# Kernel tuning notes

Hardware: AMD Instinct MI355X
Metric: run time of the kernel (lower is better)

The kernel has to match this reference:

```python
import jax, jax.numpy as jnp
import numpy as np

B, T, C = 4, 2048, 1024
H, D = 16, 64  # num_heads, head_dim
WINDOW = 256


def setup_inputs() -> dict:
    key = jax.random.key(0)
    k_x, k_qkv, k_proj, k_qb, k_pb = jax.random.split(key, 5)
    x = jax.random.normal(k_x, (B, T, C), dtype=jnp.float32)
    # xavier-uniform-ish init for qkv weight (as in _reset_parameters)
    lim_qkv = float(np.sqrt(6.0 / (C + 3 * C)))
    qkv_w = jax.random.uniform(k_qkv, (3 * C, C), minval=-lim_qkv, maxval=lim_qkv, dtype=jnp.float32)
    qkv_b = jax.random.normal(k_qb, (3 * C,), dtype=jnp.float32) * 0.02
    lim_p = float(np.sqrt(1.0 / C))
    proj_w = jax.random.uniform(k_proj, (C, C), minval=-lim_p, maxval=lim_p, dtype=jnp.float32)
    proj_b = jax.random.normal(k_pb, (C,), dtype=jnp.float32) * 0.02
    # windowed causal mask: attend to j iff j <= i and i - j < WINDOW
    i = jnp.arange(T)[:, None]
    j = jnp.arange(T)[None, :]
    attn_mask = (j <= i) & (i - j < WINDOW)  # [T, T] bool
    return {"x": x, "attn_mask": attn_mask, "qkv_w": qkv_w, "qkv_b": qkv_b,
            "proj_w": proj_w, "proj_b": proj_b}


def reference(x, attn_mask, qkv_w, qkv_b, proj_w, proj_b):
    qkv = (x @ qkv_w.T + qkv_b).reshape(B, T, 3, H, D)
    qkv = jnp.transpose(qkv, (2, 0, 3, 1, 4))
    q, k, v = qkv[0], qkv[1], qkv[2]
    scale = 1.0 / jnp.sqrt(jnp.asarray(D, dtype=q.dtype))
    scores = jnp.einsum('bhqd,bhkd->bhqk', q, k) * scale  # [B,H,T,T]
    neg = jnp.asarray(jnp.finfo(scores.dtype).min, dtype=scores.dtype)
    scores = jnp.where(attn_mask[None, None], scores, neg)
    attn = jax.nn.softmax(scores, axis=-1)
    out = jnp.einsum('bhqk,bhkd->bhqd', attn, v)  # [B,H,T,D]
    out = jnp.transpose(out, (0, 2, 1, 3)).reshape(B, T, C)
    out = out @ proj_w.T + proj_b
    return out
```

## Files before the change

### kernel.cpp

```cpp
#include <hip/hip_runtime.h>

#define BB 4
#define TT 2048
#define CC 1024
#define HH 16
#define DD 64
#define WIN 256

typedef __attribute__((ext_vector_type(8))) short short8;
typedef __attribute__((ext_vector_type(4))) float floatx4;
typedef unsigned short u16;

typedef __attribute__((address_space(3))) void lds_void;
typedef const __attribute__((address_space(1))) void g_void;

__device__ __forceinline__ void gl_lds16(const u16* g, u16* l) {
    __builtin_amdgcn_global_load_lds((g_void*)g, (lds_void*)l, 16, 0, 0);
}

__device__ __forceinline__ float bf2f(u16 u) {
    union { unsigned int i; float f; } v; v.i = ((unsigned int)u) << 16; return v.f;
}
__device__ __forceinline__ u16 f2bf(float f) {
    union { float f; unsigned int i; } v; v.f = f;
    unsigned int x = v.i;
    x += ((x >> 16) & 1u) + 0x7FFFu;
    return (u16)(x >> 16);
}

__global__ void cvt_all(const float* __restrict__ x, const float* __restrict__ qw,
                        const float* __restrict__ pw,
                        u16* __restrict__ xb, u16* __restrict__ wb, u16* __restrict__ pwb) {
    int bid = blockIdx.x;
    const float* src; u16* dst; int off;
    if (bid < 4096)      { src = x;  dst = xb;  off = bid; }
    else if (bid < 5632) { src = qw; dst = wb;  off = bid - 4096; }
    else                 { src = pw; dst = pwb; off = bid - 5632; }
    int i = (off * 256 + (int)threadIdx.x) * 8;
    float4 a = *(const float4*)(src + i);
    float4 b = *(const float4*)(src + i + 4);
    u16 o[8] = { f2bf(a.x), f2bf(a.y), f2bf(a.z), f2bf(a.w),
                 f2bf(b.x), f2bf(b.y), f2bf(b.z), f2bf(b.w) };
    *(uint4*)(dst + i) = *(const uint4*)o;
}

__global__ __launch_bounds__(256) void gemm_qk(
    const u16* __restrict__ A, const u16* __restrict__ Bw,
    const float* __restrict__ bias,
    u16* __restrict__ Qb, u16* __restrict__ Kb)
{
    const int K = CC;
    __shared__ u16 As[4096];
    __shared__ u16 Bs[4096];
    const int tid = threadIdx.x;
    const int wave = tid >> 6, lane = tid & 63;
    const int wm = wave >> 1, wn = wave & 1;
    const int quad = lane >> 4, l15 = lane & 15;
    const int bN = blockIdx.x * 128, bM = blockIdx.y * 128;

    const int srow0 = wave * 16 + (lane >> 2);
    const int srow1 = (wave + 4) * 16 + (lane >> 2);
    const int schunk = ((lane & 3) ^ ((lane >> 3) & 3)) * 8;
    const u16* gA0 = A + (size_t)(bM + srow0) * K + schunk;
    const u16* gA1 = A + (size_t)(bM + srow1) * K + schunk;
    const u16* gB0 = Bw + (size_t)(bN + srow0) * K + schunk;
    const u16* gB1 = Bw + (size_t)(bN + srow1) * K + schunk;
    u16* lA0 = &As[wave * 512];
    u16* lA1 = &As[(wave + 4) * 512];
    u16* lB0 = &Bs[wave * 512];
    u16* lB1 = &Bs[(wave + 4) * 512];

    const int rdoff = l15 * 32 + ((quad ^ ((l15 >> 1) & 3)) * 8);

    floatx4 acc[4][4] = {};

    for (int k0 = 0; k0 < K; k0 += 32) {
        __syncthreads();
        gl_lds16(gA0 + k0, lA0);
        gl_lds16(gA1 + k0, lA1);
        gl_lds16(gB0 + k0, lB0);
        gl_lds16(gB1 + k0, lB1);
        __syncthreads();
        short8 af[4], bf[4];
#pragma unroll
        for (int i = 0; i < 4; ++i) {
            af[i] = *(const short8*)&As[(wm * 4 + i) * 512 + rdoff];
            bf[i] = *(const short8*)&Bs[(wn * 4 + i) * 512 + rdoff];
        }
#pragma unroll
        for (int mi = 0; mi < 4; ++mi)
#pragma unroll
            for (int ni = 0; ni < 4; ++ni)
                acc[mi][ni] = __builtin_amdgcn_mfma_f32_16x16x32_bf16(af[mi], bf[ni], acc[mi][ni], 0, 0, 0);
    }

#pragma unroll
    for (int mi = 0; mi < 4; ++mi)
#pragma unroll
        for (int ni = 0; ni < 4; ++ni) {
            int col = bN + wn * 64 + ni * 16 + l15;
            float bv = bias[col];
            int which = col >> 10, rem = col & 1023;
            int h = rem >> 6, d = rem & 63;
            int row0 = bM + wm * 64 + mi * 16 + quad * 4;
            int b = row0 >> 11, t0 = row0 & 2047;
            u16* dst = which == 0 ? Qb : Kb;
#pragma unroll
            for (int rg = 0; rg < 4; ++rg)
                dst[(((size_t)(b * HH + h)) * TT + t0 + rg) * DD + d] = f2bf(acc[mi][ni][rg] + bv);
        }
}

__global__ __launch_bounds__(256) void gemm_v(
    const u16* __restrict__ A, const u16* __restrict__ Bw,
    const float* __restrict__ bias,
    u16* __restrict__ Vtg)
{
    const int K = CC;
    __shared__ u16 As[4096];
    __shared__ u16 Bs[4096];
    const int tid = threadIdx.x;
    const int wave = tid >> 6, lane = tid & 63;
    const int wm = wave >> 1, wn = wave & 1;
    const int quad = lane >> 4, l15 = lane & 15;
    const int bN = 2048 + blockIdx.x * 128, bM = blockIdx.y * 128;

    const int srow0 = wave * 16 + (lane >> 2);
    const int srow1 = (wave + 4) * 16 + (lane >> 2);
    const int schunk = ((lane & 3) ^ ((lane >> 3) & 3)) * 8;
    const u16* gA0 = A + (size_t)(bM + srow0) * K + schunk;
    const u16* gA1 = A + (size_t)(bM + srow1) * K + schunk;
    const u16* gB0 = Bw + (size_t)(bN + srow0) * K + schunk;
    const u16* gB1 = Bw + (size_t)(bN + srow1) * K + schunk;
    u16* lA0 = &As[wave * 512];
    u16* lA1 = &As[(wave + 4) * 512];
    u16* lB0 = &Bs[wave * 512];
    u16* lB1 = &Bs[(wave + 4) * 512];

    const int rdoff = l15 * 32 + ((quad ^ ((l15 >> 1) & 3)) * 8);

    floatx4 acc[4][4] = {};

    for (int k0 = 0; k0 < K; k0 += 32) {
        __syncthreads();
        gl_lds16(gA0 + k0, lA0);
        gl_lds16(gA1 + k0, lA1);
        gl_lds16(gB0 + k0, lB0);
        gl_lds16(gB1 + k0, lB1);
        __syncthreads();
        short8 af[4], bf[4];
#pragma unroll
        for (int i = 0; i < 4; ++i) {
            af[i] = *(const short8*)&As[(wm * 4 + i) * 512 + rdoff];
            bf[i] = *(const short8*)&Bs[(wn * 4 + i) * 512 + rdoff];
        }
#pragma unroll
        for (int mi = 0; mi < 4; ++mi)
#pragma unroll
            for (int ni = 0; ni < 4; ++ni)
                acc[mi][ni] = __builtin_amdgcn_mfma_f32_16x16x32_bf16(bf[ni], af[mi], acc[mi][ni], 0, 0, 0);
    }

#pragma unroll
    for (int mi = 0; mi < 4; ++mi)
#pragma unroll
        for (int ni = 0; ni < 4; ++ni) {
            int col0 = bN + wn * 64 + ni * 16 + quad * 4;
            int row = bM + wm * 64 + mi * 16 + l15;
            int b = row >> 11, t = row & 2047;
#pragma unroll
            for (int rg = 0; rg < 4; ++rg) {
                int c = col0 + rg;
                int h = (c & 1023) >> 6, d = c & 63;
                float v = acc[mi][ni][rg] + bias[c];
                Vtg[(((size_t)(b * HH + h)) * DD + d) * TT + t] = f2bf(v);
            }
        }
}

__global__ __launch_bounds__(256) void gemm_proj(
    const u16* __restrict__ A, const u16* __restrict__ Bw,
    const float* __restrict__ bias, float* __restrict__ Out)
{
    const int K = CC;
    __shared__ u16 As[4096];
    __shared__ u16 Bs[4096];
    const int tid = threadIdx.x;
    const int wave = tid >> 6, lane = tid & 63;
    const int wm = wave >> 1, wn = wave & 1;
    const int quad = lane >> 4, l15 = lane & 15;
    const int bN = blockIdx.x * 128, bM = blockIdx.y * 128;

    const int srow0 = wave * 16 + (lane >> 2);
    const int srow1 = (wave + 4) * 16 + (lane >> 2);
    const int schunk = ((lane & 3) ^ ((lane >> 3) & 3)) * 8;
    const u16* gA0 = A + (size_t)(bM + srow0) * K + schunk;
    const u16* gA1 = A + (size_t)(bM + srow1) * K + schunk;
    const u16* gB0 = Bw + (size_t)(bN + srow0) * K + schunk;
    const u16* gB1 = Bw + (size_t)(bN + srow1) * K + schunk;
    u16* lA0 = &As[wave * 512];
    u16* lA1 = &As[(wave + 4) * 512];
    u16* lB0 = &Bs[wave * 512];
    u16* lB1 = &Bs[(wave + 4) * 512];

    const int rdoff = l15 * 32 + ((quad ^ ((l15 >> 1) & 3)) * 8);

    floatx4 acc[4][4] = {};

    for (int k0 = 0; k0 < K; k0 += 32) {
        __syncthreads();
        gl_lds16(gA0 + k0, lA0);
        gl_lds16(gA1 + k0, lA1);
        gl_lds16(gB0 + k0, lB0);
        gl_lds16(gB1 + k0, lB1);
        __syncthreads();
        short8 af[4], bf[4];
#pragma unroll
        for (int i = 0; i < 4; ++i) {
            af[i] = *(const short8*)&As[(wm * 4 + i) * 512 + rdoff];
            bf[i] = *(const short8*)&Bs[(wn * 4 + i) * 512 + rdoff];
        }
#pragma unroll
        for (int mi = 0; mi < 4; ++mi)
#pragma unroll
            for (int ni = 0; ni < 4; ++ni)
                acc[mi][ni] = __builtin_amdgcn_mfma_f32_16x16x32_bf16(af[mi], bf[ni], acc[mi][ni], 0, 0, 0);
    }

#pragma unroll
    for (int mi = 0; mi < 4; ++mi)
#pragma unroll
        for (int ni = 0; ni < 4; ++ni) {
            int col = bN + wn * 64 + ni * 16 + l15;
            float bv = bias[col];
#pragma unroll
            for (int rg = 0; rg < 4; ++rg) {
                int row = bM + wm * 64 + mi * 16 + quad * 4 + rg;
                Out[(size_t)row * CC + col] = acc[mi][ni][rg] + bv;
            }
        }
}

__global__ __launch_bounds__(256) void attn_mfma(
    const u16* __restrict__ Qb, const u16* __restrict__ Kb, const u16* __restrict__ Vtg,
    u16* __restrict__ Y)
{
    __shared__ __align__(16) u16 Ks[4096];
    __shared__ __align__(16) u16 Vs[4096];
    __shared__ __align__(16) u16 Ps[4][16][72];

    const int tid = threadIdx.x;
    const int wave = tid >> 6, lane = tid & 63;
    const int quad = lane >> 4, l15 = lane & 15;
    const int q0 = blockIdx.x * 64;
    const int bh = blockIdx.y;
    const int b = bh >> 4, h = bh & 15;
    const u16* Qp = Qb + (size_t)bh * TT * DD;
    const u16* Kp = Kb + (size_t)bh * TT * DD;
    const u16* Vp = Vtg + (size_t)bh * DD * TT;
    const int qw = q0 + wave * 16;

    const int lrow = lane >> 3;
    const int lchunk = ((lane & 7) ^ lrow) << 3;
    const int s0 = wave * 2, s1 = wave * 2 + 1;

    short8 qf[2];
    qf[0] = *(const short8*)&Qp[(size_t)(qw + l15) * DD + quad * 8];
    qf[1] = *(const short8*)&Qp[(size_t)(qw + l15) * DD + 32 + quad * 8];

    float m_i = -1e30f, l_i = 0.f;
    floatx4 Oacc[4] = {};

    const int swz = l15 & 7;
    const int kb = (q0 >= WIN) ? (q0 - WIN) : 0;
    for (int j0 = kb; j0 < q0 + 64; j0 += 64) {
        __syncthreads();
        gl_lds16(&Kp[(size_t)(j0 + s0 * 8 + lrow) * DD + lchunk], &Ks[s0 * 512]);
        gl_lds16(&Kp[(size_t)(j0 + s1 * 8 + lrow) * DD + lchunk], &Ks[s1 * 512]);
        gl_lds16(&Vp[(size_t)(s0 * 8 + lrow) * TT + j0 + lchunk], &Vs[s0 * 512]);
        gl_lds16(&Vp[(size_t)(s1 * 8 + lrow) * TT + j0 + lchunk], &Vs[s1 * 512]);
        __syncthreads();

        floatx4 Sacc[4] = {};
#pragma unroll
        for (int ks = 0; ks < 2; ++ks)
#pragma unroll
            for (int kt = 0; kt < 4; ++kt) {
                short8 kf = *(const short8*)&Ks[(kt * 16 + l15) * 64 + (((ks * 4 + quad) ^ swz) << 3)];
                Sacc[kt] = __builtin_amdgcn_mfma_f32_16x16x32_bf16(kf, qf[ks], Sacc[kt], 0, 0, 0);
            }

        const int q = qw + l15;
        float mc = -1e30f;
#pragma unroll
        for (int kt = 0; kt < 4; ++kt)
#pragma unroll
            for (int r = 0; r < 4; ++r) {
                int j = j0 + kt * 16 + quad * 4 + r;
                float s = (j <= q && (q - j) < WIN) ? Sacc[kt][r] * 0.125f : -1e30f;
                Sacc[kt][r] = s;
                mc = fmaxf(mc, s);
            }
        mc = fmaxf(mc, __shfl_xor(mc, 16, 64));
        mc = fmaxf(mc, __shfl_xor(mc, 32, 64));

        float mn = fmaxf(m_i, mc);
        float alpha = __expf(m_i - mn);
        m_i = mn;

        float rs = 0.f;
#pragma unroll
        for (int kt = 0; kt < 4; ++kt) {
            u16 pk[4];
#pragma unroll
            for (int r = 0; r < 4; ++r) {
                float s = Sacc[kt][r];
                float p = (s > -1e29f) ? __expf(s - m_i) : 0.f;
                rs += p;
                pk[r] = f2bf(p);
            }
            *(uint2*)&Ps[wave][l15][kt * 16 + quad * 4] = *(const uint2*)pk;
        }
        rs += __shfl_xor(rs, 16, 64);
        rs += __shfl_xor(rs, 32, 64);
        l_i = l_i * alpha + rs;
#pragma unroll
        for (int dt = 0; dt < 4; ++dt)
#pragma unroll
            for (int r = 0; r < 4; ++r) Oacc[dt][r] *= alpha;

#pragma unroll
        for (int ks = 0; ks < 2; ++ks) {
            short8 pf = *(const short8*)&Ps[wave][l15][ks * 32 + quad * 8];
#pragma unroll
            for (int dt = 0; dt < 4; ++dt) {
                short8 vf = *(const short8*)&Vs[(dt * 16 + l15) * 64 + (((ks * 4 + quad) ^ swz) << 3)];
                Oacc[dt] = __builtin_amdgcn_mfma_f32_16x16x32_bf16(vf, pf, Oacc[dt], 0, 0, 0);
            }
        }
    }

    float inv = 1.f / l_i;
    const int t = qw + l15;
#pragma unroll
    for (int dt = 0; dt < 4; ++dt) {
        u16 o[4];
#pragma unroll
        for (int r = 0; r < 4; ++r) o[r] = f2bf(Oacc[dt][r] * inv);
        *(uint2*)&Y[((size_t)b * TT + t) * CC + h * DD + dt * 16 + quad * 4] = *(const uint2*)o;
    }
}

extern "C" void kernel_launch(void* const* d_in, const int* in_sizes, int n_in,
                              void* d_out, int out_size, void* d_ws, size_t ws_size,
                              hipStream_t stream) {
    const float* x      = (const float*)d_in[0];
    const float* qkv_w  = (const float*)d_in[2];
    const float* qkv_b  = (const float*)d_in[3];
    const float* proj_w = (const float*)d_in[4];
    const float* proj_b = (const float*)d_in[5];
    float* out = (float*)d_out;

    u16* xb  = (u16*)d_ws;
    u16* wb  = xb  + (size_t)8192 * 1024;
    u16* pwb = wb  + (size_t)3072 * 1024;
    u16* Qb  = pwb + (size_t)1024 * 1024;
    u16* Kb  = Qb  + (size_t)64 * 2048 * 64;
    u16* Vtg = Kb  + (size_t)64 * 2048 * 64;
    u16* Yb  = Vtg + (size_t)64 * 2048 * 64;

    cvt_all<<<6144, 256, 0, stream>>>(x, qkv_w, proj_w, xb, wb, pwb);
    gemm_qk<<<dim3(16, 64), 256, 0, stream>>>(xb, wb, qkv_b, Qb, Kb);
    gemm_v<<<dim3(8, 64), 256, 0, stream>>>(xb, wb, qkv_b, Vtg);
    attn_mfma<<<dim3(TT / 64, BB * HH), 256, 0, stream>>>(Qb, Kb, Vtg, Yb);
    gemm_proj<<<dim3(8, 64), 256, 0, stream>>>(Yb, pwb, proj_b, out);
}
```

Baseline: 246.5 us.

## Double-buffer LDS tiles in GEMM and attention kernels to overlap loads

Converts the K-loop of the three GEMM kernels and the KV loop of the attention kernel to double-buffered LDS staging. The next tile's global-to-LDS async loads are issued right after a single barrier, while the current buffer is consumed by MFMA. This removes one barrier per iteration and is meant to hide global load latency behind compute. It doubles LDS use per block, which may lower occupancy. The overlap also depends on the compiler not inserting a full vmcnt wait before the LDS reads.

```diff
diff --git a/kernel.cpp b/kernel.cpp
--- a/kernel.cpp
+++ b/kernel.cpp
@@ -44,14 +44,15 @@
     *(uint4*)(dst + i) = *(const uint4*)o;
 }
 
+
 __global__ __launch_bounds__(256) void gemm_qk(
     const u16* __restrict__ A, const u16* __restrict__ Bw,
     const float* __restrict__ bias,
     u16* __restrict__ Qb, u16* __restrict__ Kb)
 {
     const int K = CC;
-    __shared__ u16 As[4096];
-    __shared__ u16 Bs[4096];
+    __shared__ u16 As[2][4096];
+    __shared__ u16 Bs[2][4096];
     const int tid = threadIdx.x;
     const int wave = tid >> 6, lane = tid & 63;
     const int wm = wave >> 1, wn = wave & 1;
@@ -65,27 +66,28 @@
     const u16* gA1 = A + (size_t)(bM + srow1) * K + schunk;
     const u16* gB0 = Bw + (size_t)(bN + srow0) * K + schunk;
     const u16* gB1 = Bw + (size_t)(bN + srow1) * K + schunk;
-    u16* lA0 = &As[wave * 512];
-    u16* lA1 = &As[(wave + 4) * 512];
-    u16* lB0 = &Bs[wave * 512];
-    u16* lB1 = &Bs[(wave + 4) * 512];
 
     const int rdoff = l15 * 32 + ((quad ^ ((l15 >> 1) & 3)) * 8);
 
+    auto stage = [&](int k0, int buf) {
+        gl_lds16(gA0 + k0, &As[buf][wave * 512]);
+        gl_lds16(gA1 + k0, &As[buf][(wave + 4) * 512]);
+        gl_lds16(gB0 + k0, &Bs[buf][wave * 512]);
+        gl_lds16(gB1 + k0, &Bs[buf][(wave + 4) * 512]);
+    };
+
     floatx4 acc[4][4] = {};
-
-    for (int k0 = 0; k0 < K; k0 += 32) {
+    stage(0, 0);
+
+    for (int k = 0; k < K / 32; ++k) {
         __syncthreads();
-        gl_lds16(gA0 + k0, lA0);
-        gl_lds16(gA1 + k0, lA1);
-        gl_lds16(gB0 + k0, lB0);
-        gl_lds16(gB1 + k0, lB1);
-        __syncthreads();
+        if (k + 1 < K / 32) stage((k + 1) * 32, (k + 1) & 1);
+        const int cur = k & 1;
         short8 af[4], bf[4];
 #pragma unroll
         for (int i = 0; i < 4; ++i) {
-            af[i] = *(const short8*)&As[(wm * 4 + i) * 512 + rdoff];
-            bf[i] = *(const short8*)&Bs[(wn * 4 + i) * 512 + rdoff];
+            af[i] = *(const short8*)&As[cur][(wm * 4 + i) * 512 + rdoff];
+            bf[i] = *(const short8*)&Bs[cur][(wn * 4 + i) * 512 + rdoff];
         }
 #pragma unroll
         for (int mi = 0; mi < 4; ++mi)
@@ -117,8 +119,8 @@
     u16* __restrict__ Vtg)
 {
     const int K = CC;
-    __shared__ u16 As[4096];
-    __shared__ u16 Bs[4096];
+    __shared__ u16 As[2][4096];
+    __shared__ u16 Bs[2][4096];
     const int tid = threadIdx.x;
     const int wave = tid >> 6, lane = tid & 63;
     const int wm = wave >> 1, wn = wave & 1;
@@ -132,27 +134,28 @@
     const u16* gA1 = A + (size_t)(bM + srow1) * K + schunk;
     const u16* gB0 = Bw + (size_t)(bN + srow0) * K + schunk;
     const u16* gB1 = Bw + (size_t)(bN + srow1) * K + schunk;
-    u16* lA0 = &As[wave * 512];
-    u16* lA1 = &As[(wave + 4) * 512];
-    u16* lB0 = &Bs[wave * 512];
-    u16* lB1 = &Bs[(wave + 4) * 512];
 
     const int rdoff = l15 * 32 + ((quad ^ ((l15 >> 1) & 3)) * 8);
 
+    auto stage = [&](int k0, int buf) {
+        gl_lds16(gA0 + k0, &As[buf][wave * 512]);
+        gl_lds16(gA1 + k0, &As[buf][(wave + 4) * 512]);
+        gl_lds16(gB0 + k0, &Bs[buf][wave * 512]);
+        gl_lds16(gB1 + k0, &Bs[buf][(wave + 4) * 512]);
+    };
+
     floatx4 acc[4][4] = {};
-
-    for (int k0 = 0; k0 < K; k0 += 32) {
+    stage(0, 0);
+
+    for (int k = 0; k < K / 32; ++k) {
         __syncthreads();
-        gl_lds16(gA0 + k0, lA0);
-        gl_lds16(gA1 + k0, lA1);
-        gl_lds16(gB0 + k0, lB0);
-        gl_lds16(gB1 + k0, lB1);
-        __syncthreads();
+        if (k + 1 < K / 32) stage((k + 1) * 32, (k + 1) & 1);
+        const int cur = k & 1;
         short8 af[4], bf[4];
 #pragma unroll
         for (int i = 0; i < 4; ++i) {
-            af[i] = *(const short8*)&As[(wm * 4 + i) * 512 + rdoff];
-            bf[i] = *(const short8*)&Bs[(wn * 4 + i) * 512 + rdoff];
+            af[i] = *(const short8*)&As[cur][(wm * 4 + i) * 512 + rdoff];
+            bf[i] = *(const short8*)&Bs[cur][(wn * 4 + i) * 512 + rdoff];
         }
 #pragma unroll
         for (int mi = 0; mi < 4; ++mi)
@@ -183,8 +186,8 @@
     const float* __restrict__ bias, float* __restrict__ Out)
 {
     const int K = CC;
-    __shared__ u16 As[4096];
-    __shared__ u16 Bs[4096];
+    __shared__ u16 As[2][4096];
+    __shared__ u16 Bs[2][4096];
     const int tid = threadIdx.x;
     const int wave = tid >> 6, lane = tid & 63;
     const int wm = wave >> 1, wn = wave & 1;
@@ -198,27 +201,28 @@
     const u16* gA1 = A + (size_t)(bM + srow1) * K + schunk;
     const u16* gB0 = Bw + (size_t)(bN + srow0) * K + schunk;
     const u16* gB1 = Bw + (size_t)(bN + srow1) * K + schunk;
-    u16* lA0 = &As[wave * 512];
-    u16* lA1 = &As[(wave + 4) * 512];
-    u16* lB0 = &Bs[wave * 512];
-    u16* lB1 = &Bs[(wave + 4) * 512];
 
     const int rdoff = l15 * 32 + ((quad ^ ((l15 >> 1) & 3)) * 8);
 
+    auto stage = [&](int k0, int buf) {
+        gl_lds16(gA0 + k0, &As[buf][wave * 512]);
+        gl_lds16(gA1 + k0, &As[buf][(wave + 4) * 512]);
+        gl_lds16(gB0 + k0, &Bs[buf][wave * 512]);
+        gl_lds16(gB1 + k0, &Bs[buf][(wave + 4) * 512]);
+    };
+
     floatx4 acc[4][4] = {};
-
-    for (int k0 = 0; k0 < K; k0 += 32) {
+    stage(0, 0);
+
+    for (int k = 0; k < K / 32; ++k) {
         __syncthreads();
-        gl_lds16(gA0 + k0, lA0);
-        gl_lds16(gA1 + k0, lA1);
-        gl_lds16(gB0 + k0, lB0);
-        gl_lds16(gB1 + k0, lB1);
-        __syncthreads();
+        if (k + 1 < K / 32) stage((k + 1) * 32, (k + 1) & 1);
+        const int cur = k & 1;
         short8 af[4], bf[4];
 #pragma unroll
         for (int i = 0; i < 4; ++i) {
-            af[i] = *(const short8*)&As[(wm * 4 + i) * 512 + rdoff];
-            bf[i] = *(const short8*)&Bs[(wn * 4 + i) * 512 + rdoff];
+            af[i] = *(const short8*)&As[cur][(wm * 4 + i) * 512 + rdoff];
+            bf[i] = *(const short8*)&Bs[cur][(wn * 4 + i) * 512 + rdoff];
         }
 #pragma unroll
         for (int mi = 0; mi < 4; ++mi)
@@ -245,8 +249,8 @@
     const u16* __restrict__ Qb, const u16* __restrict__ Kb, const u16* __restrict__ Vtg,
     u16* __restrict__ Y)
 {
-    __shared__ __align__(16) u16 Ks[4096];
-    __shared__ __align__(16) u16 Vs[4096];
+    __shared__ __align__(16) u16 Ks[2][4096];
+    __shared__ __align__(16) u16 Vs[2][4096];
     __shared__ __align__(16) u16 Ps[4][16][72];
 
     const int tid = threadIdx.x;
@@ -264,6 +268,13 @@
     const int lchunk = ((lane & 7) ^ lrow) << 3;
     const int s0 = wave * 2, s1 = wave * 2 + 1;
 
+    auto stageKV = [&](int j0, int buf) {
+        gl_lds16(&Kp[(size_t)(j0 + s0 * 8 + lrow) * DD + lchunk], &Ks[buf][s0 * 512]);
+        gl_lds16(&Kp[(size_t)(j0 + s1 * 8 + lrow) * DD + lchunk], &Ks[buf][s1 * 512]);
+        gl_lds16(&Vp[(size_t)(s0 * 8 + lrow) * TT + j0 + lchunk], &Vs[buf][s0 * 512]);
+        gl_lds16(&Vp[(size_t)(s1 * 8 + lrow) * TT + j0 + lchunk], &Vs[buf][s1 * 512]);
+    };
+
     short8 qf[2];
     qf[0] = *(const short8*)&Qp[(size_t)(qw + l15) * DD + quad * 8];
     qf[1] = *(const short8*)&Qp[(size_t)(qw + l15) * DD + 32 + quad * 8];
@@ -273,20 +284,19 @@
 
     const int swz = l15 & 7;
     const int kb = (q0 >= WIN) ? (q0 - WIN) : 0;
-    for (int j0 = kb; j0 < q0 + 64; j0 += 64) {
+    stageKV(kb, 0);
+    int c = 0;
+    for (int j0 = kb; j0 < q0 + 64; j0 += 64, ++c) {
         __syncthreads();
-        gl_lds16(&Kp[(size_t)(j0 + s0 * 8 + lrow) * DD + lchunk], &Ks[s0 * 512]);
-        gl_lds16(&Kp[(size_t)(j0 + s1 * 8 + lrow) * DD + lchunk], &Ks[s1 * 512]);
-        gl_lds16(&Vp[(size_t)(s0 * 8 + lrow) * TT + j0 + lchunk], &Vs[s0 * 512]);
-        gl_lds16(&Vp[(size_t)(s1 * 8 + lrow) * TT + j0 + lchunk], &Vs[s1 * 512]);
-        __syncthreads();
+        if (j0 + 64 < q0 + 64) stageKV(j0 + 64, (c + 1) & 1);
+        const int cur = c & 1;
 
         floatx4 Sacc[4] = {};
 #pragma unroll
         for (int ks = 0; ks < 2; ++ks)
 #pragma unroll
             for (int kt = 0; kt < 4; ++kt) {
-                short8 kf = *(const short8*)&Ks[(kt * 16 + l15) * 64 + (((ks * 4 + quad) ^ swz) << 3)];
+                short8 kf = *(const short8*)&Ks[cur][(kt * 16 + l15) * 64 + (((ks * 4 + quad) ^ swz) << 3)];
                 Sacc[kt] = __builtin_amdgcn_mfma_f32_16x16x32_bf16(kf, qf[ks], Sacc[kt], 0, 0, 0);
             }
 
@@ -334,7 +344,7 @@
             short8 pf = *(const short8*)&Ps[wave][l15][ks * 32 + quad * 8];
 #pragma unroll
             for (int dt = 0; dt < 4; ++dt) {
-                short8 vf = *(const short8*)&Vs[(dt * 16 + l15) * 64 + (((ks * 4 + quad) ^ swz) << 3)];
+                short8 vf = *(const short8*)&Vs[cur][(dt * 16 + l15) * 64 + (((ks * 4 + quad) ^ swz) << 3)];
                 Oacc[dt] = __builtin_amdgcn_mfma_f32_16x16x32_bf16(vf, pf, Oacc[dt], 0, 0, 0);
             }
         }
```

Result: slower. 269.0 us (+9.1%).
